# Optimization experiments

Measured on AMD Instinct MI355X. Metric: run time of the kernel, lower is better.

## Reference

```python
import jax, jax.numpy as jnp
import numpy as np

BETA = 0.25
ENT_MULT = 0.1
COMMIT_MULT = 0.1


def setup_inputs() -> dict:
    key = jax.random.key(0)
    z = jax.random.normal(key, (64, 13, 128, 128), dtype=jnp.float32)
    return {"z": z}


def reference(z):
    B, C, H, W = z.shape
    # (B,C,H,W) -> (B,H,W,C) -> (N,C)
    zf = jnp.transpose(z, (0, 2, 3, 1)).reshape(-1, C)
    # binary sign quantization (>0 -> +1, else -1) with straight-through estimator
    q = jnp.where(zf > 0, 1.0, -1.0).astype(zf.dtype)
    z_q = zf + jax.lax.stop_gradient(q - zf)
    # Categorical over logits [-(z-1)^2, -(z+1)^2] per latent dim; shape (N,C,2)
    logits = jnp.stack([-(zf - 1.0) ** 2, -(zf + 1.0) ** 2], axis=-1)
    logp = jax.nn.log_softmax(logits, axis=-1)
    p = jnp.exp(logp)
    entropy = jnp.mean(-(p * logp).sum(-1))          # per-sample entropy, averaged
    mean_prob = p.mean(0)                              # (C,2), rows already sum to 1
    mean_entropy = jnp.mean(-(mean_prob * jnp.log(mean_prob)).sum(-1))
    # commitment loss (both directions, beta-weighted)
    commit_loss = jnp.mean((jax.lax.stop_gradient(z_q) - zf) ** 2) \
        + BETA * jnp.mean((z_q - jax.lax.stop_gradient(zf)) ** 2)
    # back to (B,C,H,W)
    z_q4 = jnp.transpose(z_q.reshape(B, H, W, C), (0, 3, 1, 2))
    # bit-pack indices: MSB = channel 0
    powers = (2 ** jnp.arange(C - 1, -1, -1)).astype(jnp.float32)  # (C,)
    indices = (powers.reshape(1, -1, 1, 1) * (z_q4 > 0).astype(jnp.float32)) \
        .sum(axis=1, keepdims=True).astype(jnp.int32)              # (B,1,H,W)
    return (z_q4,
            commit_loss * COMMIT_MULT,
            (entropy - mean_entropy) * ENT_MULT,
            indices)
```

## Files before the change

### kernel.cpp

```cpp
#include <hip/hip_runtime.h>
#include <math.h>

constexpr int B = 64;
constexpr int C = 13;
constexpr int HW = 128 * 128;
constexpr long long NTOT = (long long)B * C * HW;
constexpr long long NSAMP = (long long)B * HW;

constexpr long long COMMIT_OFF = NTOT;
constexpr long long ENT_OFF = NTOT + 1;
constexpr long long IDX_OFF = NTOT + 2;

constexpr int THREADS = 256;
constexpr int VEC = 4;
constexpr int CHUNK = THREADS * VEC;
constexpr int BLOCKS_PER_B = HW / CHUNK;
constexpr int NBLK = B * BLOCKS_PER_B;
constexpr int NACC = 15;
constexpr int SLOT = 16;

typedef float nfloat4 __attribute__((ext_vector_type(4)));

__global__ __launch_bounds__(THREADS, 4) void lfq_main(const float* __restrict__ z,
                                                       float* __restrict__ out,
                                                       float* __restrict__ part) {
    constexpr float kLog2e4 = 5.7707801635558535f;
    constexpr float kLn2 = 0.6931471805599453f;

    const int bid = blockIdx.x;
    const int b = bid / BLOCKS_PER_B;
    const int j = bid % BLOCKS_PER_B;
    const int hw0 = j * CHUNK + (int)threadIdx.x * VEC;

    float cm_s = 0.0f;
    float ent_s = 0.0f;
    float p0_s[C];
#pragma unroll
    for (int c = 0; c < C; ++c) p0_s[c] = 0.0f;
    int idx[VEC] = {0, 0, 0, 0};

    const float* zb = z + (size_t)b * C * HW + hw0;
    float* zq = out + (size_t)b * C * HW + hw0;

#pragma unroll
    for (int c = 0; c < C; ++c) {
        const float4 v = *reinterpret_cast<const float4*>(zb + (size_t)c * HW);
        float zz[VEC] = {v.x, v.y, v.z, v.w};
        float qq[VEC];
#pragma unroll
        for (int k = 0; k < VEC; ++k) {
            const float zv = zz[k];
            const bool pos = (zv > 0.0f);
            qq[k] = pos ? 1.0f : -1.0f;
            const float az = fabsf(zv);
            const float dm = az - 1.0f;
            cm_s = fmaf(dm, dm, cm_s);
            const float e = __builtin_amdgcn_exp2f(-kLog2e4 * az);
            const float ope = 1.0f + e;
            const float sp = __builtin_amdgcn_logf(ope) * kLn2;
            const float ps = e * __builtin_amdgcn_rcpf(ope);
            ent_s += fmaf(4.0f * az, ps, sp);
            p0_s[c] += pos ? (1.0f - ps) : ps;
            if (pos) idx[k] |= (1 << (C - 1 - c));
        }
        nfloat4 qv = {qq[0], qq[1], qq[2], qq[3]};
        __builtin_nontemporal_store(qv, reinterpret_cast<nfloat4*>(zq + (size_t)c * HW));
    }

    nfloat4 fi = {(float)idx[0], (float)idx[1], (float)idx[2], (float)idx[3]};
    __builtin_nontemporal_store(fi, reinterpret_cast<nfloat4*>(out + IDX_OFF + (size_t)b * HW + hw0));

    float vals[NACC];
    vals[0] = cm_s;
    vals[1] = ent_s;
#pragma unroll
    for (int c = 0; c < C; ++c) vals[2 + c] = p0_s[c];
#pragma unroll
    for (int off = 32; off > 0; off >>= 1) {
#pragma unroll
        for (int k = 0; k < NACC; ++k) vals[k] += __shfl_down(vals[k], off);
    }
    __shared__ float red[THREADS / 64][NACC];
    const int wave = threadIdx.x >> 6;
    const int lane = threadIdx.x & 63;
    if (lane == 0) {
#pragma unroll
        for (int k = 0; k < NACC; ++k) red[wave][k] = vals[k];
    }
    __syncthreads();
    if (threadIdx.x < NACC) {
        float s = 0.0f;
#pragma unroll
        for (int w = 0; w < THREADS / 64; ++w) s += red[w][threadIdx.x];
        part[(size_t)bid * SLOT + threadIdx.x] = s;
    }
}

__global__ __launch_bounds__(NBLK) void lfq_final(const float* __restrict__ part,
                                                  float* __restrict__ out) {
    const int t = threadIdx.x;
    float vals[NACC];
    const float* p = part + (size_t)t * SLOT;
#pragma unroll
    for (int k = 0; k < NACC; ++k) vals[k] = p[k];
#pragma unroll
    for (int off = 32; off > 0; off >>= 1) {
#pragma unroll
        for (int k = 0; k < NACC; ++k) vals[k] += __shfl_down(vals[k], off);
    }
    __shared__ float red[NBLK / 64][NACC];
    const int wave = t >> 6;
    const int lane = t & 63;
    if (lane == 0) {
#pragma unroll
        for (int k = 0; k < NACC; ++k) red[wave][k] = vals[k];
    }
    __syncthreads();
    __shared__ double accs[NACC];
    if (t < NACC) {
        double s = 0.0;
#pragma unroll
        for (int w = 0; w < NBLK / 64; ++w) s += (double)red[w][t];
        accs[t] = s;
    }
    __syncthreads();
    __shared__ double ment[C];
    if (t < C) {
        const double mp0 = accs[2 + t] / (double)NSAMP;
        const double mp1 = 1.0 - mp0;
        ment[t] = -(mp0 * log(mp0) + mp1 * log(mp1));
    }
    __syncthreads();
    if (t == 0) {
        double me = 0.0;
#pragma unroll
        for (int c = 0; c < C; ++c) me += ment[c];
        me /= (double)C;
        const double commit = accs[0] / (double)NTOT;
        const double ent = accs[1] / (double)NTOT;
        out[COMMIT_OFF] = (float)(0.1 * 1.25 * commit);
        out[ENT_OFF] = (float)(0.1 * (ent - me));
    }
}

extern "C" void kernel_launch(void* const* d_in, const int* in_sizes, int n_in,
                              void* d_out, int out_size, void* d_ws, size_t ws_size,
                              hipStream_t stream) {
    const float* z = (const float*)d_in[0];
    float* out = (float*)d_out;
    float* part = (float*)d_ws;

    lfq_main<<<NBLK, THREADS, 0, stream>>>(z, out, part);
    lfq_final<<<1, NBLK, 0, stream>>>(part, out);
}
```

Before: 110.4 us.

## Fuse final reduction into main kernel via last-block atomic counter

Removes the separate single-block finalize kernel. Each block publishes its partial sums with atomic stores and bumps a global counter, and the last block to arrive reads every partial and computes the losses. This saves one kernel launch and the gap between kernels, but adds a memset of the counter before each launch and an acq_rel atomic in every block.

Result: slower. 167.4 us (+51.7%).

```diff
diff --git a/kernel.cpp b/kernel.cpp
--- a/kernel.cpp
+++ b/kernel.cpp
@@ -19,13 +19,18 @@
 constexpr int NACC = 15;
 constexpr int SLOT = 16;
 
+constexpr size_t COUNTER_BYTE_OFF = (size_t)NBLK * SLOT * sizeof(float);
+
 typedef float nfloat4 __attribute__((ext_vector_type(4)));
 
 __global__ __launch_bounds__(THREADS, 4) void lfq_main(const float* __restrict__ z,
                                                        float* __restrict__ out,
-                                                       float* __restrict__ part) {
+                                                       float* __restrict__ part,
+                                                       unsigned int* __restrict__ counter) {
     constexpr float kLog2e4 = 5.7707801635558535f;
     constexpr float kLn2 = 0.6931471805599453f;
+
+    __shared__ float red[THREADS / 64][NACC];
 
     const int bid = blockIdx.x;
     const int b = bid / BLOCKS_PER_B;
@@ -80,7 +85,6 @@
 #pragma unroll
         for (int k = 0; k < NACC; ++k) vals[k] += __shfl_down(vals[k], off);
     }
-    __shared__ float red[THREADS / 64][NACC];
     const int wave = threadIdx.x >> 6;
     const int lane = threadIdx.x & 63;
     if (lane == 0) {
@@ -92,35 +96,47 @@
         float s = 0.0f;
 #pragma unroll
         for (int w = 0; w < THREADS / 64; ++w) s += red[w][threadIdx.x];
-        part[(size_t)bid * SLOT + threadIdx.x] = s;
+        __hip_atomic_store(&part[(size_t)bid * SLOT + threadIdx.x], s,
+                           __ATOMIC_RELAXED, __HIP_MEMORY_SCOPE_AGENT);
     }
-}
 
-__global__ __launch_bounds__(NBLK) void lfq_final(const float* __restrict__ part,
-                                                  float* __restrict__ out) {
+    __shared__ int amLast;
+    __syncthreads();
+    if (threadIdx.x == 0) {
+        unsigned int old = __hip_atomic_fetch_add(counter, 1u,
+                                                  __ATOMIC_ACQ_REL, __HIP_MEMORY_SCOPE_AGENT);
+        amLast = (old == (unsigned int)(NBLK - 1));
+    }
+    __syncthreads();
+    if (!amLast) return;
+
     const int t = threadIdx.x;
-    float vals[NACC];
-    const float* p = part + (size_t)t * SLOT;
+    float fv[NACC];
 #pragma unroll
-    for (int k = 0; k < NACC; ++k) vals[k] = p[k];
+    for (int k = 0; k < NACC; ++k) fv[k] = 0.0f;
+#pragma unroll
+    for (int s4 = 0; s4 < NBLK / THREADS; ++s4) {
+        const float* p = part + (size_t)(s4 * THREADS + t) * SLOT;
+#pragma unroll
+        for (int k = 0; k < NACC; ++k)
+            fv[k] += __hip_atomic_load(&p[k], __ATOMIC_RELAXED, __HIP_MEMORY_SCOPE_AGENT);
+    }
 #pragma unroll
     for (int off = 32; off > 0; off >>= 1) {
 #pragma unroll
-        for (int k = 0; k < NACC; ++k) vals[k] += __shfl_down(vals[k], off);
+        for (int k = 0; k < NACC; ++k) fv[k] += __shfl_down(fv[k], off);
     }
-    __shared__ float red[NBLK / 64][NACC];
-    const int wave = t >> 6;
-    const int lane = t & 63;
+    __syncthreads();
     if (lane == 0) {
 #pragma unroll
-        for (int k = 0; k < NACC; ++k) red[wave][k] = vals[k];
+        for (int k = 0; k < NACC; ++k) red[wave][k] = fv[k];
     }
     __syncthreads();
     __shared__ double accs[NACC];
     if (t < NACC) {
         double s = 0.0;
 #pragma unroll
-        for (int w = 0; w < NBLK / 64; ++w) s += (double)red[w][t];
+        for (int w = 0; w < THREADS / 64; ++w) s += (double)red[w][t];
         accs[t] = s;
     }
     __syncthreads();
@@ -149,7 +165,8 @@
     const float* z = (const float*)d_in[0];
     float* out = (float*)d_out;
     float* part = (float*)d_ws;
+    unsigned int* counter = (unsigned int*)((char*)d_ws + COUNTER_BYTE_OFF);
 
-    lfq_main<<<NBLK, THREADS, 0, stream>>>(z, out, part);
-    lfq_final<<<1, NBLK, 0, stream>>>(part, out);
+    hipMemsetAsync((void*)counter, 0, sizeof(unsigned int), stream);
+    lfq_main<<<NBLK, THREADS, 0, stream>>>(z, out, part, counter);
 }
```
